# Performance work log

Measured on AMD Instinct MI355X. Metric: run time of the kernel, lower is better.

Reference implementation:

```python
import jax, jax.numpy as jnp
import numpy as np

N_USERS = 50000
N_ITEMS = 40000
D = 64
E = 1_000_000
NB = 3       # behaviors
L = 2        # GCN layers per behavior
B = 8192
N_NODES = (N_USERS + 1) + (N_ITEMS + 1)
REG_WEIGHT = 0.01
CL_TEMP = 0.1
BPR_GAMMA = 1e-10


def setup_inputs() -> dict:
    key = jax.random.key(0)
    k1, k2, k3, k4, k5 = jax.random.split(key, 5)
    user_emb = jax.random.normal(k1, (N_USERS + 1, D), jnp.float32) * 0.1
    item_emb = jax.random.normal(k2, (N_ITEMS + 1, D), jnp.float32) * 0.1
    gcn_w = jax.random.normal(k3, (NB, L, D, D), jnp.float32) * 0.1
    gcn_b = jnp.zeros((NB, L, D), jnp.float32)
    edge_index = jax.random.randint(k4, (NB, 2, E), 0, N_NODES, dtype=jnp.int64)
    batch_data = jax.random.randint(k5, (B, NB, 3), 0, 40000, dtype=jnp.int64)
    return {"user_emb": user_emb, "item_emb": item_emb, "gcn_w": gcn_w,
            "gcn_b": gcn_b, "edge_index": edge_index, "batch_data": batch_data}


def gcn_layer(x, edge_index, W, b):
    # PyG GCNConv(add_self_loops=False): h = x @ W; out[col] += norm * h[row]; out += b
    row, col = edge_index[0], edge_index[1]
    n = x.shape[0]
    deg = jnp.zeros((n,), x.dtype).at[col].add(1.0)
    dinv = jnp.where(deg > 0, jax.lax.rsqrt(jnp.maximum(deg, 1.0)), 0.0)
    norm = dinv[row] * dinv[col]                    # [E]
    h = x @ W                                       # [N, D]
    msg = h[row] * norm[:, None]                    # [E, D] gather
    out = jnp.zeros_like(x).at[col].add(msg)        # scatter-add
    return out + b


def _cos(a, b):
    num = jnp.sum(a * b, axis=-1)
    den = jnp.maximum(jnp.linalg.norm(a, axis=-1) * jnp.linalg.norm(b, axis=-1), 1e-8)
    return num / den


def reference(user_emb, item_emb, gcn_w, gcn_b, edge_index, batch_data):
    total = jnp.concatenate([user_emb, item_emb], axis=0)   # [N_NODES, D]
    total_loss = jnp.float32(0.0)
    te = total
    for bi in range(NB):
        # gcn propagate for this behavior (eval: dropout is identity)
        le = te
        for l in range(L):
            le = gcn_layer(le, edge_index[bi], gcn_w[bi, l], gcn_b[bi, l])
        # F.normalize(dim=-1)
        le = le / jnp.maximum(jnp.linalg.norm(le, axis=-1, keepdims=True), 1e-12)
        te = le + te
        # losses for this behavior
        users = batch_data[:, bi, 0]
        items = batch_data[:, bi, 1:]                        # [B, 2]
        ue = te[:N_USERS + 1]
        ie = te[N_USERS + 1:]
        uf = ue[users]                                       # [B, D]
        itf = ie[items]                                      # [B, 2, D]
        pos, neg = itf[:, 0], itf[:, 1]
        # info-nce (cross-entropy over [pos, neg] cosine sims, label 0)
        logits = jnp.stack([_cos(uf, pos), _cos(uf, neg)], axis=1) / CL_TEMP
        cl_loss = jnp.mean(-jax.nn.log_softmax(logits, axis=-1)[:, 0])
        # BPR loss (weight per behavior = 1.0)
        scores = jnp.sum(uf[:, None, :] * itf, axis=2)       # [B, 2]
        bpr = jnp.mean(-jnp.log(BPR_GAMMA + jax.nn.sigmoid(scores[:, 0] - scores[:, 1])))
        total_loss = total_loss + bpr + cl_loss
    # EmbLoss: sum of L2 norms of the raw embedding tables / last table's rows
    emb_loss = (jnp.linalg.norm(user_emb) + jnp.linalg.norm(item_emb)) / item_emb.shape[0]
    return total_loss + REG_WEIGHT * emb_loss
```

## Files before the change

kernel.cpp:

```cpp
#include <hip/hip_runtime.h>
#include <hip/hip_fp16.h>
#include <math.h>

#define NU 50001
#define NI 40001
#define NNODES 90002
#define DD 64
#define EE 1000000
#define NBB 3
#define LL 2
#define BB 8192
#define STRIDE 40
#define QS 16.0f
#define QS2 64.0f
#define T4U (NU * 16)
#define T4T (NNODES * 16)
#define NBIN 352
#define NPAD (NBIN * 256)
#define CHUNK 4096
#define NBLK 245

__device__ __forceinline__ void acc8(float4& A, float4& Bv, uint2 w) {
    A.x  += __builtin_amdgcn_cvt_f32_fp8((int)w.x, 0);
    A.y  += __builtin_amdgcn_cvt_f32_fp8((int)w.x, 1);
    A.z  += __builtin_amdgcn_cvt_f32_fp8((int)w.x, 2);
    A.w  += __builtin_amdgcn_cvt_f32_fp8((int)w.x, 3);
    Bv.x += __builtin_amdgcn_cvt_f32_fp8((int)w.y, 0);
    Bv.y += __builtin_amdgcn_cvt_f32_fp8((int)w.y, 1);
    Bv.z += __builtin_amdgcn_cvt_f32_fp8((int)w.y, 2);
    Bv.w += __builtin_amdgcn_cvt_f32_fp8((int)w.y, 3);
}

__global__ __launch_bounds__(512) void k_scatp(const int* __restrict__ edge,
                                               unsigned* __restrict__ binbufC,
                                               unsigned* __restrict__ Htab) {
    __shared__ unsigned posc[NBIN];
    __shared__ unsigned sc[512];
    __shared__ unsigned lb[CHUNK];
    int bi = blockIdx.y, blk = blockIdx.x, tid = threadIdx.x;
    for (int i = tid; i < NBIN; i += 512) posc[i] = 0;
    __syncthreads();
    const int* rowp = edge + (size_t)bi * 2 * EE;
    const int* colp = rowp + EE;
    int base = blk * CHUNK;
    unsigned pk[8], bn[8];
    #pragma unroll
    for (int k = 0; k < 8; k++) {
        int e = base + k * 512 + tid;
        if (e < EE) {
            unsigned c = (unsigned)colp[e];
            pk[k] = ((c & 255u) << 17) | (unsigned)rowp[e];
            bn[k] = c >> 8;
            atomicAdd(&posc[bn[k]], 1u);
        } else bn[k] = 0xFFFFFFFFu;
    }
    __syncthreads();
    unsigned v = (tid < NBIN) ? posc[tid] : 0u;
    sc[tid] = v;
    __syncthreads();
    #pragma unroll
    for (int o = 1; o < 512; o <<= 1) {
        unsigned u = (tid >= o) ? sc[tid - o] : 0u;
        __syncthreads();
        sc[tid] += u;
        __syncthreads();
    }
    if (tid < NBIN) {
        unsigned excl = sc[tid] - v;
        Htab[(((size_t)bi * 2 + 0) * NBLK + blk) * NBIN + tid] = v;
        Htab[(((size_t)bi * 2 + 1) * NBLK + blk) * NBIN + tid] = excl;
        posc[tid] = excl;
    }
    __syncthreads();
    #pragma unroll
    for (int k = 0; k < 8; k++) {
        if (bn[k] != 0xFFFFFFFFu) {
            unsigned pos = atomicAdd(&posc[bn[k]], 1u);
            lb[pos] = pk[k];
        }
    }
    __syncthreads();
    uint4* d4 = (uint4*)(binbufC + ((size_t)bi * NBLK + blk) * CHUNK);
    const uint4* s4 = (const uint4*)lb;
    #pragma unroll
    for (int k = 0; k < CHUNK / 4 / 512; k++)
        d4[k * 512 + tid] = s4[k * 512 + tid];
}

__global__ __launch_bounds__(1024) void k_transp(const unsigned* __restrict__ in, unsigned* __restrict__ out) {
    __shared__ unsigned t[32][33];
    int z = blockIdx.z;
    const unsigned* I = in + (size_t)z * NBLK * NBIN;
    unsigned* O = out + (size_t)z * NBIN * NBLK;
    int bin0 = blockIdx.x * 32, blk0 = blockIdx.y * 32;
    int tx = threadIdx.x & 31, ty = threadIdx.x >> 5;
    int bin = bin0 + tx, blk = blk0 + ty;
    if (blk < NBLK && bin < NBIN) t[ty][tx] = I[(size_t)blk * NBIN + bin];
    __syncthreads();
    int obin = bin0 + ty, oblk = blk0 + tx;
    if (obin < NBIN && oblk < NBLK) O[(size_t)obin * NBLK + oblk] = t[tx][ty];
}

__global__ __launch_bounds__(256) void k_bucket(const unsigned* __restrict__ HtabT,
                                                const unsigned* __restrict__ binbufC,
                                                unsigned* __restrict__ cnt3, unsigned* __restrict__ bucket3) {
    __shared__ unsigned lb[256 * STRIDE];
    __shared__ unsigned cl[256];
    __shared__ unsigned so[NBLK + 1];
    __shared__ unsigned bo[NBLK];
    __shared__ unsigned sc[256];
    int bi = blockIdx.y, bin = blockIdx.x, tid = threadIdx.x;
    cl[tid] = 0;
    unsigned v = 0;
    if (tid < NBLK) {
        v = HtabT[(((size_t)bi * 2 + 0) * NBIN + bin) * NBLK + tid];
        bo[tid] = HtabT[(((size_t)bi * 2 + 1) * NBIN + bin) * NBLK + tid];
    }
    sc[tid] = v;
    __syncthreads();
    #pragma unroll
    for (int o = 1; o < 256; o <<= 1) {
        unsigned u = (tid >= o) ? sc[tid - o] : 0u;
        __syncthreads();
        sc[tid] += u;
        __syncthreads();
    }
    if (tid == 0) so[0] = 0;
    if (tid < NBLK) so[tid + 1] = sc[tid];
    __syncthreads();
    unsigned T = so[NBLK];
    for (unsigned i = tid; i < T; i += 256) {
        int lo = 0, hi = NBLK;
        while (hi - lo > 1) { int mid = (lo + hi) >> 1; if (so[mid] <= i) lo = mid; else hi = mid; }
        unsigned w = binbufC[((size_t)bi * NBLK + lo) * CHUNK + bo[lo] + (i - so[lo])];
        unsigned c = w >> 17;
        unsigned pos = atomicAdd(&cl[c], 1u);
        if (pos < STRIDE) lb[c * STRIDE + pos] = w & 0x1FFFFu;
    }
    __syncthreads();
    cnt3[(size_t)bi * NPAD + (size_t)bin * 256 + tid] = cl[tid];
    uint4* dst = (uint4*)(bucket3 + (size_t)bi * NPAD * STRIDE + (size_t)bin * 256 * STRIDE);
    const uint4* srcl = (const uint4*)lb;
    #pragma unroll
    for (int k = 0; k < (256 * STRIDE / 4) / 256; k++)
        dst[k * 256 + tid] = srcl[k * 256 + tid];
}

__global__ __launch_bounds__(256) void k_dinv3(const unsigned* __restrict__ cnt3, float* __restrict__ dinv3) {
    int i = blockIdx.x * 256 + threadIdx.x;
    if (i < NBB * NPAD) { unsigned d = cnt3[i]; dinv3[i] = d ? rsqrtf((float)d) : 0.f; }
}

__global__ __launch_bounds__(256) void k_wprep(const float* __restrict__ gcn_w, const float* __restrict__ gcn_b,
                                               float* __restrict__ W01, float* __restrict__ bW) {
    __shared__ float w0[64 * 64], w1[64 * 64];
    int bi = blockIdx.x, tid = threadIdx.x;
    const float* W0 = gcn_w + ((size_t)bi * 2 + 0) * 4096;
    const float* W1 = gcn_w + ((size_t)bi * 2 + 1) * 4096;
    #pragma unroll
    for (int k = 0; k < 4; k++) {
        ((float4*)w0)[k * 256 + tid] = ((const float4*)W0)[k * 256 + tid];
        ((float4*)w1)[k * 256 + tid] = ((const float4*)W1)[k * 256 + tid];
    }
    __syncthreads();
    int i = tid & 63;
    int jq = tid >> 6;
    float acc[16];
    #pragma unroll
    for (int j = 0; j < 16; j++) acc[j] = 0.f;
    for (int k = 0; k < 64; k++) {
        float a = w0[i * 64 + k];
        #pragma unroll
        for (int j = 0; j < 16; j++) acc[j] += a * w1[k * 64 + jq * 16 + j];
    }
    float* O = W01 + (size_t)bi * 4096 + (size_t)i * 64 + jq * 16;
    #pragma unroll
    for (int j = 0; j < 16; j++) O[j] = acc[j];
    if (tid < 64) {
        const float* b0 = gcn_b + ((size_t)bi * 2 + 0) * 64;
        float a = 0.f;
        for (int k = 0; k < 64; k++) a += b0[k] * w1[k * 64 + tid];
        bW[bi * 64 + tid] = a;
    }
}

__global__ __launch_bounds__(256) void k_init(const float* __restrict__ user_emb,
                                              const float* __restrict__ item_emb,
                                              const unsigned* __restrict__ cnt0,
                                              float* __restrict__ te, unsigned* __restrict__ X8a,
                                              float* __restrict__ scal) {
    int i0 = blockIdx.x * 256 + threadIdx.x;
    int stride = gridDim.x * 256;
    float su = 0.f, si = 0.f;
    const float4* u4 = (const float4*)user_emb;
    const float4* i4 = (const float4*)item_emb;
    float4* t4 = (float4*)te;
    for (int i = i0; i < T4T; i += stride) {
        float4 v;
        if (i < T4U) { v = u4[i]; su += v.x * v.x + v.y * v.y + v.z * v.z + v.w * v.w; }
        else         { v = i4[i - T4U]; si += v.x * v.x + v.y * v.y + v.z * v.z + v.w * v.w; }
        t4[i] = v;
        unsigned d = cnt0[i >> 4];
        float q = (d ? rsqrtf((float)d) : 0.f) * QS;
        int p0 = __builtin_amdgcn_cvt_pk_fp8_f32(v.x * q, v.y * q, 0, false);
        p0 = __builtin_amdgcn_cvt_pk_fp8_f32(v.z * q, v.w * q, p0, true);
        X8a[i] = (unsigned)p0;
    }
    #pragma unroll
    for (int o = 32; o > 0; o >>= 1) { su += __shfl_down(su, o); si += __shfl_down(si, o); }
    __shared__ float lsu[4], lsi[4];
    int w = threadIdx.x >> 6;
    if ((threadIdx.x & 63) == 0) { lsu[w] = su; lsi[w] = si; }
    __syncthreads();
    if (threadIdx.x == 0) {
        atomicAdd(scal + 1, lsu[0] + lsu[1] + lsu[2] + lsu[3]);
        atomicAdd(scal + 2, lsi[0] + lsi[1] + lsi[2] + lsi[3]);
    }
}

__global__ __launch_bounds__(256) void k_agg1(const unsigned* __restrict__ cnt,
                                              const unsigned* __restrict__ bucket,
                                              const uint2* __restrict__ X8in,
                                              const float* __restrict__ dinv,
                                              unsigned* __restrict__ X8out,
                                              float* __restrict__ sarr) {
    int t = blockIdx.x * 256 + threadIdx.x;
    int r = t >> 6;
    if (r >= NNODES) return;
    int lane = t & 63;
    int j2 = lane & 7;
    int hw = lane >> 3;
    unsigned d = cnt[r];
    unsigned dc = d < STRIDE ? d : STRIDE;
    const unsigned* bk = bucket + (size_t)r * STRIDE;
    unsigned a0 = (hw +  0 < dc) ? bk[hw +  0] : (unsigned)NNODES;
    unsigned a1 = (hw +  8 < dc) ? bk[hw +  8] : (unsigned)NNODES;
    unsigned a2 = (hw + 16 < dc) ? bk[hw + 16] : (unsigned)NNODES;
    unsigned a3 = (hw + 24 < dc) ? bk[hw + 24] : (unsigned)NNODES;
    uint2 w0 = X8in[(size_t)a0 * 8 + j2];
    uint2 w1 = X8in[(size_t)a1 * 8 + j2];
    uint2 w2 = X8in[(size_t)a2 * 8 + j2];
    uint2 w3 = X8in[(size_t)a3 * 8 + j2];
    float sa = dinv[a0] + dinv[a1] + dinv[a2] + dinv[a3];
    float4 A = {0.f, 0.f, 0.f, 0.f}, Bv = {0.f, 0.f, 0.f, 0.f};
    acc8(A, Bv, w0); acc8(A, Bv, w1); acc8(A, Bv, w2); acc8(A, Bv, w3);
    for (unsigned i = hw + 32; i < dc; i += 8) {
        unsigned a = bk[i];
        uint2 w = X8in[(size_t)a * 8 + j2];
        acc8(A, Bv, w);
        sa += dinv[a];
    }
    #pragma unroll
    for (int o = 8; o <= 32; o <<= 1) {
        A.x  += __shfl_xor(A.x, o);  A.y  += __shfl_xor(A.y, o);
        A.z  += __shfl_xor(A.z, o);  A.w  += __shfl_xor(A.w, o);
        Bv.x += __shfl_xor(Bv.x, o); Bv.y += __shfl_xor(Bv.y, o);
        Bv.z += __shfl_xor(Bv.z, o); Bv.w += __shfl_xor(Bv.w, o);
        sa   += __shfl_xor(sa, o);
    }
    float dv = dinv[r];
    if (hw == 0) {
        float q2 = QS2 * dv * dv * (1.0f / QS);
        int p0 = __builtin_amdgcn_cvt_pk_fp8_f32(A.x * q2, A.y * q2, 0, false);
        p0 = __builtin_amdgcn_cvt_pk_fp8_f32(A.z * q2, A.w * q2, p0, true);
        int p1 = __builtin_amdgcn_cvt_pk_fp8_f32(Bv.x * q2, Bv.y * q2, 0, false);
        p1 = __builtin_amdgcn_cvt_pk_fp8_f32(Bv.z * q2, Bv.w * q2, p1, true);
        uint2 pw; pw.x = (unsigned)p0; pw.y = (unsigned)p1;
        ((uint2*)X8out)[(size_t)r * 8 + j2] = pw;
        if (j2 == 0) sarr[r] = dv * sa;
    }
}

__global__ __launch_bounds__(256) void k_agg(const unsigned* __restrict__ cnt,
                                             const unsigned* __restrict__ bucket,
                                             const uint2* __restrict__ X8in,
                                             __half* __restrict__ agg) {
    int t = blockIdx.x * 256 + threadIdx.x;
    int r = t >> 6;
    if (r >= NNODES) return;
    int lane = t & 63;
    int j2 = lane & 7;
    int hw = lane >> 3;
    unsigned d = cnt[r];
    unsigned dc = d < STRIDE ? d : STRIDE;
    const unsigned* bk = bucket + (size_t)r * STRIDE;
    unsigned a0 = (hw +  0 < dc) ? bk[hw +  0] : (unsigned)NNODES;
    unsigned a1 = (hw +  8 < dc) ? bk[hw +  8] : (unsigned)NNODES;
    unsigned a2 = (hw + 16 < dc) ? bk[hw + 16] : (unsigned)NNODES;
    unsigned a3 = (hw + 24 < dc) ? bk[hw + 24] : (unsigned)NNODES;
    uint2 w0 = X8in[(size_t)a0 * 8 + j2];
    uint2 w1 = X8in[(size_t)a1 * 8 + j2];
    uint2 w2 = X8in[(size_t)a2 * 8 + j2];
    uint2 w3 = X8in[(size_t)a3 * 8 + j2];
    float4 A = {0.f, 0.f, 0.f, 0.f}, Bv = {0.f, 0.f, 0.f, 0.f};
    acc8(A, Bv, w0); acc8(A, Bv, w1); acc8(A, Bv, w2); acc8(A, Bv, w3);
    for (unsigned i = hw + 32; i < dc; i += 8) {
        uint2 w = X8in[(size_t)bk[i] * 8 + j2];
        acc8(A, Bv, w);
    }
    #pragma unroll
    for (int o = 8; o <= 32; o <<= 1) {
        A.x  += __shfl_xor(A.x, o);  A.y  += __shfl_xor(A.y, o);
        A.z  += __shfl_xor(A.z, o);  A.w  += __shfl_xor(A.w, o);
        Bv.x += __shfl_xor(Bv.x, o); Bv.y += __shfl_xor(Bv.y, o);
        Bv.z += __shfl_xor(Bv.z, o); Bv.w += __shfl_xor(Bv.w, o);
    }
    if (hw == 0) {
        union { __half2 h[4]; float4 f; } u;
        u.h[0] = __floats2half2_rn(A.x, A.y);
        u.h[1] = __floats2half2_rn(A.z, A.w);
        u.h[2] = __floats2half2_rn(Bv.x, Bv.y);
        u.h[3] = __floats2half2_rn(Bv.z, Bv.w);
        ((float4*)agg)[(size_t)r * 8 + j2] = u.f;
    }
}

__global__ __launch_bounds__(256) void k_gemmE(const __half* __restrict__ agg, const float* __restrict__ W01,
                                               const float* __restrict__ bW, const float* __restrict__ b1,
                                               const unsigned* __restrict__ cnt, const float* __restrict__ sarr,
                                               float* __restrict__ te, unsigned* __restrict__ X8out,
                                               const unsigned* __restrict__ cnt_next) {
    __shared__ float ws[64 * 64];
    __shared__ float xs[16][64];
    int tid = threadIdx.x;
    #pragma unroll
    for (int q = 0; q < 4; q++)
        ((float4*)ws)[tid + q * 256] = ((const float4*)W01)[tid + q * 256];
    int r0 = blockIdx.x * 16;
    {
        int rr = r0 + (tid >> 4);
        int cc = (tid & 15) * 4;
        if (rr < NNODES) {
            uint2 u = ((const uint2*)agg)[(size_t)rr * 16 + (tid & 15)];
            union { unsigned u; __half2 h; } c0, c1;
            c0.u = u.x; c1.u = u.y;
            float2 f0 = __half22float2(c0.h);
            float2 f1 = __half22float2(c1.h);
            xs[tid >> 4][cc + 0] = f0.x; xs[tid >> 4][cc + 1] = f0.y;
            xs[tid >> 4][cc + 2] = f1.x; xs[tid >> 4][cc + 3] = f1.y;
        }
    }
    __syncthreads();
    int rloc = tid >> 4;
    int j = tid & 15;
    int d4 = j * 4;
    int row = r0 + rloc;
    if (row >= NNODES) return;
    float4 acc = {0.f, 0.f, 0.f, 0.f};
    #pragma unroll
    for (int k = 0; k < 64; k++) {
        float xv = xs[rloc][k];
        float4 wv = *(const float4*)&ws[k * 64 + d4];
        acc.x += xv * wv.x; acc.y += xv * wv.y;
        acc.z += xv * wv.z; acc.w += xv * wv.w;
    }
    unsigned d = cnt[row];
    float m = (d ? rsqrtf((float)d) : 0.f) * (1.0f / QS2);
    float sv = sarr[row];
    float4 bwv = ((const float4*)bW)[j];
    float4 b1v = ((const float4*)b1)[j];
    float vx = acc.x * m + sv * bwv.x + b1v.x;
    float vy = acc.y * m + sv * bwv.y + b1v.y;
    float vz = acc.z * m + sv * bwv.z + b1v.z;
    float vw = acc.w * m + sv * bwv.w + b1v.w;
    float s = vx * vx + vy * vy + vz * vz + vw * vw;
    #pragma unroll
    for (int o = 1; o <= 8; o <<= 1) s += __shfl_xor(s, o);
    float scale = 1.f / fmaxf(sqrtf(s), 1e-12f);
    float4* te4 = (float4*)te;
    float4 old = te4[(size_t)row * 16 + j];
    old.x += vx * scale; old.y += vy * scale;
    old.z += vz * scale; old.w += vw * scale;
    te4[(size_t)row * 16 + j] = old;
    if (X8out) {
        unsigned dn = cnt_next[row];
        float q = (dn ? rsqrtf((float)dn) : 0.f) * QS;
        int p0 = __builtin_amdgcn_cvt_pk_fp8_f32(old.x * q, old.y * q, 0, false);
        p0 = __builtin_amdgcn_cvt_pk_fp8_f32(old.z * q, old.w * q, p0, true);
        X8out[(size_t)row * 16 + j] = (unsigned)p0;
    }
}

__global__ __launch_bounds__(256) void k_loss(const float* __restrict__ te, const int* __restrict__ batch,
                                              int bi, float* __restrict__ acc) {
    int t = blockIdx.x * 256 + threadIdx.x;
    int s = t >> 6;
    int lane = t & 63;
    if (s >= BB) return;
    const int* bd = &batch[s * (NBB * 3) + bi * 3];
    int u = bd[0], p = bd[1], n = bd[2];
    float uv = te[(size_t)u * DD + lane];
    float pv = te[(size_t)(NU + p) * DD + lane];
    float nv = te[(size_t)(NU + n) * DD + lane];
    float d_up = uv * pv, d_un = uv * nv;
    float s_u = uv * uv, s_p = pv * pv, s_n = nv * nv;
    for (int o = 32; o > 0; o >>= 1) {
        d_up += __shfl_xor(d_up, o);
        d_un += __shfl_xor(d_un, o);
        s_u  += __shfl_xor(s_u, o);
        s_p  += __shfl_xor(s_p, o);
        s_n  += __shfl_xor(s_n, o);
    }
    __shared__ float part[4];
    if (lane == 0) {
        float cosp = d_up / fmaxf(sqrtf(s_u) * sqrtf(s_p), 1e-8f);
        float cosn = d_un / fmaxf(sqrtf(s_u) * sqrtf(s_n), 1e-8f);
        float cl = log1pf(expf((cosn - cosp) * 10.0f));
        float sig = 1.f / (1.f + expf(-(d_up - d_un)));
        float bpr = -logf(1e-10f + sig);
        part[(threadIdx.x >> 6) & 3] = cl + bpr;
    }
    __syncthreads();
    if (threadIdx.x == 0)
        atomicAdd(acc, (part[0] + part[1] + part[2] + part[3]) * (1.0f / BB));
}

__global__ void k_final(const float* __restrict__ scal, float* __restrict__ out) {
    if (threadIdx.x == 0 && blockIdx.x == 0)
        out[0] = scal[0] + 0.01f * (sqrtf(scal[1]) + sqrtf(scal[2])) / 40001.0f;
}

extern "C" void kernel_launch(void* const* d_in, const int* in_sizes, int n_in,
                              void* d_out, int out_size, void* d_ws, size_t ws_size,
                              hipStream_t stream) {
    const float* user_emb = (const float*)d_in[0];
    const float* item_emb = (const float*)d_in[1];
    const float* gcn_w    = (const float*)d_in[2];
    const float* gcn_b    = (const float*)d_in[3];
    const int*   edge_idx = (const int*)d_in[4];
    const int*   batch    = (const int*)d_in[5];
    float* out = (float*)d_out;

    char* ws = (char*)d_ws;
    size_t off = 0;
    auto alloc = [&](size_t bytes) {
        void* p = ws + off;
        off = (off + bytes + 511) & ~(size_t)511;
        return p;
    };
    float*    te      = (float*)alloc((size_t)NNODES * DD * sizeof(float));
    __half*   agg     = (__half*)alloc((size_t)NNODES * DD * sizeof(__half));
    unsigned* X8a     = (unsigned*)alloc((size_t)(NNODES + 1) * 16 * sizeof(unsigned));
    unsigned* X8b     = (unsigned*)alloc((size_t)(NNODES + 1) * 16 * sizeof(unsigned));
    unsigned* cnt3    = (unsigned*)alloc((size_t)NBB * NPAD * sizeof(unsigned));
    float*    dinv3   = (float*)alloc((size_t)NBB * NPAD * sizeof(float));
    unsigned* bucket3 = (unsigned*)alloc((size_t)NBB * NPAD * STRIDE * sizeof(unsigned));
    unsigned* binbufC = (unsigned*)alloc((size_t)NBB * NBLK * CHUNK * sizeof(unsigned));
    unsigned* Htab    = (unsigned*)alloc((size_t)NBB * 2 * NBLK * NBIN * sizeof(unsigned));
    unsigned* HtabT   = (unsigned*)alloc((size_t)NBB * 2 * NBIN * NBLK * sizeof(unsigned));
    float*    W01     = (float*)alloc((size_t)NBB * 4096 * sizeof(float));
    float*    bW      = (float*)alloc((size_t)NBB * 64 * sizeof(float));
    float*    sarr    = (float*)alloc((size_t)NNODES * sizeof(float));
    float*    scal    = (float*)alloc(64 * sizeof(float));

    hipMemsetAsync(scal, 0, 64 * sizeof(float), stream);
    hipMemsetAsync(X8a + (size_t)NNODES * 16, 0, 64, stream);
    hipMemsetAsync(X8b + (size_t)NNODES * 16, 0, 64, stream);

    k_scatp <<<dim3(NBLK, NBB), 512, 0, stream>>>(edge_idx, binbufC, Htab);
    k_transp<<<dim3((NBIN + 31) / 32, (NBLK + 31) / 32, NBB * 2), 1024, 0, stream>>>(Htab, HtabT);
    k_bucket<<<dim3(NBIN, NBB), 256, 0, stream>>>(HtabT, binbufC, cnt3, bucket3);
    k_dinv3 <<<(NBB * NPAD + 255) / 256, 256, 0, stream>>>(cnt3, dinv3);
    k_wprep <<<NBB, 256, 0, stream>>>(gcn_w, gcn_b, W01, bW);

    k_init<<<1024, 256, 0, stream>>>(user_emb, item_emb, cnt3, te, X8a, scal);

    const int gat_grid  = (NNODES * DD + 255) / 256;
    const int gemm_grid = (NNODES + 15) / 16;

    for (int bi = 0; bi < NBB; bi++) {
        const unsigned* cnt = cnt3 + (size_t)bi * NPAD;
        const float*    dnv = dinv3 + (size_t)bi * NPAD;
        const unsigned* bucket = bucket3 + (size_t)bi * NPAD * STRIDE;
        const float* b1 = gcn_b + ((size_t)bi * LL + 1) * DD;

        k_agg1<<<gat_grid, 256, 0, stream>>>(cnt, bucket, (const uint2*)X8a, dnv, X8b, sarr);
        k_agg<<<gat_grid, 256, 0, stream>>>(cnt, bucket, (const uint2*)X8b, agg);
        unsigned* x8next = (bi < NBB - 1) ? X8a : nullptr;
        const unsigned* cnt_next = cnt3 + (size_t)((bi + 1) % NBB) * NPAD;
        k_gemmE<<<gemm_grid, 256, 0, stream>>>(agg, W01 + (size_t)bi * 4096, bW + (size_t)bi * 64,
                                               b1, cnt, sarr, te, x8next, cnt_next);

        k_loss<<<(BB * 64) / 256, 256, 0, stream>>>(te, batch, bi, scal);
    }

    k_final<<<1, 64, 0, stream>>>(scal, out);
}
```

Measured before the change: 441.1 us.

## Fuse second-layer aggregation into GEMM kernel and fold dinv into bucket kernel

Merges the fp8 neighbor aggregation for the second GCN layer with the dense W01 projection, normalize and residual update into one kernel that stages 64 aggregated rows in shared memory. This removes the fp16 intermediate buffer round trip and one launch per behavior. The degree-inverse computation moves into the bucketing kernel, removing a separate launch and the rsqrt recomputation in the consumers. Each wave now gathers 16 rows serially and the block uses more shared memory, which may reduce memory-level parallelism and occupancy.

```diff
diff --git a/kernel.cpp b/kernel.cpp
--- a/kernel.cpp
+++ b/kernel.cpp
@@ -103,7 +103,8 @@
 
 __global__ __launch_bounds__(256) void k_bucket(const unsigned* __restrict__ HtabT,
                                                 const unsigned* __restrict__ binbufC,
-                                                unsigned* __restrict__ cnt3, unsigned* __restrict__ bucket3) {
+                                                unsigned* __restrict__ cnt3, float* __restrict__ dinv3,
+                                                unsigned* __restrict__ bucket3) {
     __shared__ unsigned lb[256 * STRIDE];
     __shared__ unsigned cl[256];
     __shared__ unsigned so[NBLK + 1];
@@ -138,17 +139,14 @@
         if (pos < STRIDE) lb[c * STRIDE + pos] = w & 0x1FFFFu;
     }
     __syncthreads();
-    cnt3[(size_t)bi * NPAD + (size_t)bin * 256 + tid] = cl[tid];
+    unsigned d = cl[tid];
+    cnt3[(size_t)bi * NPAD + (size_t)bin * 256 + tid] = d;
+    dinv3[(size_t)bi * NPAD + (size_t)bin * 256 + tid] = d ? rsqrtf((float)d) : 0.f;
     uint4* dst = (uint4*)(bucket3 + (size_t)bi * NPAD * STRIDE + (size_t)bin * 256 * STRIDE);
     const uint4* srcl = (const uint4*)lb;
     #pragma unroll
     for (int k = 0; k < (256 * STRIDE / 4) / 256; k++)
         dst[k * 256 + tid] = srcl[k * 256 + tid];
-}
-
-__global__ __launch_bounds__(256) void k_dinv3(const unsigned* __restrict__ cnt3, float* __restrict__ dinv3) {
-    int i = blockIdx.x * 256 + threadIdx.x;
-    if (i < NBB * NPAD) { unsigned d = cnt3[i]; dinv3[i] = d ? rsqrtf((float)d) : 0.f; }
 }
 
 __global__ __launch_bounds__(256) void k_wprep(const float* __restrict__ gcn_w, const float* __restrict__ gcn_b,
@@ -186,7 +184,7 @@
 
 __global__ __launch_bounds__(256) void k_init(const float* __restrict__ user_emb,
                                               const float* __restrict__ item_emb,
-                                              const unsigned* __restrict__ cnt0,
+                                              const float* __restrict__ dinv0,
                                               float* __restrict__ te, unsigned* __restrict__ X8a,
                                               float* __restrict__ scal) {
     int i0 = blockIdx.x * 256 + threadIdx.x;
@@ -200,8 +198,7 @@
         if (i < T4U) { v = u4[i]; su += v.x * v.x + v.y * v.y + v.z * v.z + v.w * v.w; }
         else         { v = i4[i - T4U]; si += v.x * v.x + v.y * v.y + v.z * v.z + v.w * v.w; }
         t4[i] = v;
-        unsigned d = cnt0[i >> 4];
-        float q = (d ? rsqrtf((float)d) : 0.f) * QS;
+        float q = dinv0[i >> 4] * QS;
         int p0 = __builtin_amdgcn_cvt_pk_fp8_f32(v.x * q, v.y * q, 0, false);
         p0 = __builtin_amdgcn_cvt_pk_fp8_f32(v.z * q, v.w * q, p0, true);
         X8a[i] = (unsigned)p0;
@@ -271,113 +268,101 @@
     }
 }
 
-__global__ __launch_bounds__(256) void k_agg(const unsigned* __restrict__ cnt,
-                                             const unsigned* __restrict__ bucket,
-                                             const uint2* __restrict__ X8in,
-                                             __half* __restrict__ agg) {
-    int t = blockIdx.x * 256 + threadIdx.x;
-    int r = t >> 6;
-    if (r >= NNODES) return;
-    int lane = t & 63;
+__global__ __launch_bounds__(256) void k_aggGemm(const unsigned* __restrict__ cnt,
+                                                 const unsigned* __restrict__ bucket,
+                                                 const uint2* __restrict__ X8in,
+                                                 const float* __restrict__ W01,
+                                                 const float* __restrict__ bW,
+                                                 const float* __restrict__ b1,
+                                                 const float* __restrict__ dinv,
+                                                 const float* __restrict__ sarr,
+                                                 float* __restrict__ te,
+                                                 unsigned* __restrict__ X8out,
+                                                 const float* __restrict__ dinv_next) {
+    __shared__ float ws[64 * 64];
+    __shared__ float xs[64][68];
+    int tid = threadIdx.x;
+    #pragma unroll
+    for (int q = 0; q < 4; q++)
+        ((float4*)ws)[tid + q * 256] = ((const float4*)W01)[tid + q * 256];
+    int r0 = blockIdx.x * 64;
+    int u = tid >> 6;
+    int lane = tid & 63;
     int j2 = lane & 7;
     int hw = lane >> 3;
-    unsigned d = cnt[r];
-    unsigned dc = d < STRIDE ? d : STRIDE;
-    const unsigned* bk = bucket + (size_t)r * STRIDE;
-    unsigned a0 = (hw +  0 < dc) ? bk[hw +  0] : (unsigned)NNODES;
-    unsigned a1 = (hw +  8 < dc) ? bk[hw +  8] : (unsigned)NNODES;
-    unsigned a2 = (hw + 16 < dc) ? bk[hw + 16] : (unsigned)NNODES;
-    unsigned a3 = (hw + 24 < dc) ? bk[hw + 24] : (unsigned)NNODES;
-    uint2 w0 = X8in[(size_t)a0 * 8 + j2];
-    uint2 w1 = X8in[(size_t)a1 * 8 + j2];
-    uint2 w2 = X8in[(size_t)a2 * 8 + j2];
-    uint2 w3 = X8in[(size_t)a3 * 8 + j2];
-    float4 A = {0.f, 0.f, 0.f, 0.f}, Bv = {0.f, 0.f, 0.f, 0.f};
-    acc8(A, Bv, w0); acc8(A, Bv, w1); acc8(A, Bv, w2); acc8(A, Bv, w3);
-    for (unsigned i = hw + 32; i < dc; i += 8) {
-        uint2 w = X8in[(size_t)bk[i] * 8 + j2];
-        acc8(A, Bv, w);
-    }
-    #pragma unroll
-    for (int o = 8; o <= 32; o <<= 1) {
-        A.x  += __shfl_xor(A.x, o);  A.y  += __shfl_xor(A.y, o);
-        A.z  += __shfl_xor(A.z, o);  A.w  += __shfl_xor(A.w, o);
-        Bv.x += __shfl_xor(Bv.x, o); Bv.y += __shfl_xor(Bv.y, o);
-        Bv.z += __shfl_xor(Bv.z, o); Bv.w += __shfl_xor(Bv.w, o);
-    }
-    if (hw == 0) {
-        union { __half2 h[4]; float4 f; } u;
-        u.h[0] = __floats2half2_rn(A.x, A.y);
-        u.h[1] = __floats2half2_rn(A.z, A.w);
-        u.h[2] = __floats2half2_rn(Bv.x, Bv.y);
-        u.h[3] = __floats2half2_rn(Bv.z, Bv.w);
-        ((float4*)agg)[(size_t)r * 8 + j2] = u.f;
-    }
-}
-
-__global__ __launch_bounds__(256) void k_gemmE(const __half* __restrict__ agg, const float* __restrict__ W01,
-                                               const float* __restrict__ bW, const float* __restrict__ b1,
-                                               const unsigned* __restrict__ cnt, const float* __restrict__ sarr,
-                                               float* __restrict__ te, unsigned* __restrict__ X8out,
-                                               const unsigned* __restrict__ cnt_next) {
-    __shared__ float ws[64 * 64];
-    __shared__ float xs[16][64];
-    int tid = threadIdx.x;
-    #pragma unroll
-    for (int q = 0; q < 4; q++)
-        ((float4*)ws)[tid + q * 256] = ((const float4*)W01)[tid + q * 256];
-    int r0 = blockIdx.x * 16;
-    {
-        int rr = r0 + (tid >> 4);
-        int cc = (tid & 15) * 4;
-        if (rr < NNODES) {
-            uint2 u = ((const uint2*)agg)[(size_t)rr * 16 + (tid & 15)];
-            union { unsigned u; __half2 h; } c0, c1;
-            c0.u = u.x; c1.u = u.y;
-            float2 f0 = __half22float2(c0.h);
-            float2 f1 = __half22float2(c1.h);
-            xs[tid >> 4][cc + 0] = f0.x; xs[tid >> 4][cc + 1] = f0.y;
-            xs[tid >> 4][cc + 2] = f1.x; xs[tid >> 4][cc + 3] = f1.y;
-        }
-    }
-    __syncthreads();
-    int rloc = tid >> 4;
+    for (int it = 0; it < 16; ++it) {
+        int rl = it * 4 + u;
+        int r = r0 + rl;
+        unsigned d = cnt[r];
+        unsigned dc = d < STRIDE ? d : STRIDE;
+        const unsigned* bk = bucket + (size_t)r * STRIDE;
+        unsigned a0 = (hw +  0 < dc) ? bk[hw +  0] : (unsigned)NNODES;
+        unsigned a1 = (hw +  8 < dc) ? bk[hw +  8] : (unsigned)NNODES;
+        unsigned a2 = (hw + 16 < dc) ? bk[hw + 16] : (unsigned)NNODES;
+        unsigned a3 = (hw + 24 < dc) ? bk[hw + 24] : (unsigned)NNODES;
+        uint2 w0 = X8in[(size_t)a0 * 8 + j2];
+        uint2 w1 = X8in[(size_t)a1 * 8 + j2];
+        uint2 w2 = X8in[(size_t)a2 * 8 + j2];
+        uint2 w3 = X8in[(size_t)a3 * 8 + j2];
+        float4 A = {0.f, 0.f, 0.f, 0.f}, Bv = {0.f, 0.f, 0.f, 0.f};
+        acc8(A, Bv, w0); acc8(A, Bv, w1); acc8(A, Bv, w2); acc8(A, Bv, w3);
+        for (unsigned i = hw + 32; i < dc; i += 8) {
+            uint2 w = X8in[(size_t)bk[i] * 8 + j2];
+            acc8(A, Bv, w);
+        }
+        #pragma unroll
+        for (int o = 8; o <= 32; o <<= 1) {
+            A.x  += __shfl_xor(A.x, o);  A.y  += __shfl_xor(A.y, o);
+            A.z  += __shfl_xor(A.z, o);  A.w  += __shfl_xor(A.w, o);
+            Bv.x += __shfl_xor(Bv.x, o); Bv.y += __shfl_xor(Bv.y, o);
+            Bv.z += __shfl_xor(Bv.z, o); Bv.w += __shfl_xor(Bv.w, o);
+        }
+        if (hw == 0) {
+            *(float4*)&xs[rl][j2 * 8]     = A;
+            *(float4*)&xs[rl][j2 * 8 + 4] = Bv;
+        }
+    }
+    __syncthreads();
     int j = tid & 15;
+    int g = tid >> 4;
     int d4 = j * 4;
-    int row = r0 + rloc;
-    if (row >= NNODES) return;
-    float4 acc = {0.f, 0.f, 0.f, 0.f};
-    #pragma unroll
-    for (int k = 0; k < 64; k++) {
-        float xv = xs[rloc][k];
-        float4 wv = *(const float4*)&ws[k * 64 + d4];
-        acc.x += xv * wv.x; acc.y += xv * wv.y;
-        acc.z += xv * wv.z; acc.w += xv * wv.w;
-    }
-    unsigned d = cnt[row];
-    float m = (d ? rsqrtf((float)d) : 0.f) * (1.0f / QS2);
-    float sv = sarr[row];
-    float4 bwv = ((const float4*)bW)[j];
-    float4 b1v = ((const float4*)b1)[j];
-    float vx = acc.x * m + sv * bwv.x + b1v.x;
-    float vy = acc.y * m + sv * bwv.y + b1v.y;
-    float vz = acc.z * m + sv * bwv.z + b1v.z;
-    float vw = acc.w * m + sv * bwv.w + b1v.w;
-    float s = vx * vx + vy * vy + vz * vz + vw * vw;
-    #pragma unroll
-    for (int o = 1; o <= 8; o <<= 1) s += __shfl_xor(s, o);
-    float scale = 1.f / fmaxf(sqrtf(s), 1e-12f);
-    float4* te4 = (float4*)te;
-    float4 old = te4[(size_t)row * 16 + j];
-    old.x += vx * scale; old.y += vy * scale;
-    old.z += vz * scale; old.w += vw * scale;
-    te4[(size_t)row * 16 + j] = old;
-    if (X8out) {
-        unsigned dn = cnt_next[row];
-        float q = (dn ? rsqrtf((float)dn) : 0.f) * QS;
-        int p0 = __builtin_amdgcn_cvt_pk_fp8_f32(old.x * q, old.y * q, 0, false);
-        p0 = __builtin_amdgcn_cvt_pk_fp8_f32(old.z * q, old.w * q, p0, true);
-        X8out[(size_t)row * 16 + j] = (unsigned)p0;
+    #pragma unroll
+    for (int rr = 0; rr < 4; ++rr) {
+        int rl = rr * 16 + g;
+        int row = r0 + rl;
+        float4 acc = {0.f, 0.f, 0.f, 0.f};
+        #pragma unroll
+        for (int k = 0; k < 64; k++) {
+            float xv = xs[rl][k];
+            float4 wv = *(const float4*)&ws[k * 64 + d4];
+            acc.x += xv * wv.x; acc.y += xv * wv.y;
+            acc.z += xv * wv.z; acc.w += xv * wv.w;
+        }
+        if (row < NNODES) {
+            float m = dinv[row] * (1.0f / QS2);
+            float sv = sarr[row];
+            float4 bwv = ((const float4*)bW)[j];
+            float4 b1v = ((const float4*)b1)[j];
+            float vx = acc.x * m + sv * bwv.x + b1v.x;
+            float vy = acc.y * m + sv * bwv.y + b1v.y;
+            float vz = acc.z * m + sv * bwv.z + b1v.z;
+            float vw = acc.w * m + sv * bwv.w + b1v.w;
+            float s = vx * vx + vy * vy + vz * vz + vw * vw;
+            #pragma unroll
+            for (int o = 1; o <= 8; o <<= 1) s += __shfl_xor(s, o);
+            float scale = 1.f / fmaxf(sqrtf(s), 1e-12f);
+            float4* te4 = (float4*)te;
+            float4 old = te4[(size_t)row * 16 + j];
+            old.x += vx * scale; old.y += vy * scale;
+            old.z += vz * scale; old.w += vw * scale;
+            te4[(size_t)row * 16 + j] = old;
+            if (X8out) {
+                float q = dinv_next[row] * QS;
+                int p0 = __builtin_amdgcn_cvt_pk_fp8_f32(old.x * q, old.y * q, 0, false);
+                p0 = __builtin_amdgcn_cvt_pk_fp8_f32(old.z * q, old.w * q, p0, true);
+                X8out[(size_t)row * 16 + j] = (unsigned)p0;
+            }
+        }
     }
 }
 
@@ -439,7 +424,6 @@
         return p;
     };
     float*    te      = (float*)alloc((size_t)NNODES * DD * sizeof(float));
-    __half*   agg     = (__half*)alloc((size_t)NNODES * DD * sizeof(__half));
     unsigned* X8a     = (unsigned*)alloc((size_t)(NNODES + 1) * 16 * sizeof(unsigned));
     unsigned* X8b     = (unsigned*)alloc((size_t)(NNODES + 1) * 16 * sizeof(unsigned));
     unsigned* cnt3    = (unsigned*)alloc((size_t)NBB * NPAD * sizeof(unsigned));
@@ -459,14 +443,13 @@
 
     k_scatp <<<dim3(NBLK, NBB), 512, 0, stream>>>(edge_idx, binbufC, Htab);
     k_transp<<<dim3((NBIN + 31) / 32, (NBLK + 31) / 32, NBB * 2), 1024, 0, stream>>>(Htab, HtabT);
-    k_bucket<<<dim3(NBIN, NBB), 256, 0, stream>>>(HtabT, binbufC, cnt3, bucket3);
-    k_dinv3 <<<(NBB * NPAD + 255) / 256, 256, 0, stream>>>(cnt3, dinv3);
+    k_bucket<<<dim3(NBIN, NBB), 256, 0, stream>>>(HtabT, binbufC, cnt3, dinv3, bucket3);
     k_wprep <<<NBB, 256, 0, stream>>>(gcn_w, gcn_b, W01, bW);
 
-    k_init<<<1024, 256, 0, stream>>>(user_emb, item_emb, cnt3, te, X8a, scal);
-
-    const int gat_grid  = (NNODES * DD + 255) / 256;
-    const int gemm_grid = (NNODES + 15) / 16;
+    k_init<<<1024, 256, 0, stream>>>(user_emb, item_emb, dinv3, te, X8a, scal);
+
+    const int gat_grid = (NNODES * DD + 255) / 256;
+    const int agm_grid = (NNODES + 63) / 64;
 
     for (int bi = 0; bi < NBB; bi++) {
         const unsigned* cnt = cnt3 + (size_t)bi * NPAD;
@@ -475,11 +458,11 @@
         const float* b1 = gcn_b + ((size_t)bi * LL + 1) * DD;
 
         k_agg1<<<gat_grid, 256, 0, stream>>>(cnt, bucket, (const uint2*)X8a, dnv, X8b, sarr);
-        k_agg<<<gat_grid, 256, 0, stream>>>(cnt, bucket, (const uint2*)X8b, agg);
         unsigned* x8next = (bi < NBB - 1) ? X8a : nullptr;
-        const unsigned* cnt_next = cnt3 + (size_t)((bi + 1) % NBB) * NPAD;
-        k_gemmE<<<gemm_grid, 256, 0, stream>>>(agg, W01 + (size_t)bi * 4096, bW + (size_t)bi * 64,
-                                               b1, cnt, sarr, te, x8next, cnt_next);
+        const float* dnv_next = dinv3 + (size_t)((bi + 1) % NBB) * NPAD;
+        k_aggGemm<<<agm_grid, 256, 0, stream>>>(cnt, bucket, (const uint2*)X8b,
+                                                W01 + (size_t)bi * 4096, bW + (size_t)bi * 64, b1,
+                                                dnv, sarr, te, x8next, dnv_next);
 
         k_loss<<<(BB * 64) / 256, 256, 0, stream>>>(te, batch, bi, scal);
     }
```

Measured after the change: 503.3 us. +14.1%, slower.
